# Performance work log

Measured on AMD Instinct MI355X. Metric: run time of the kernel, lower is better.

## Reference

```python
import jax, jax.numpy as jnp
import numpy as np

D_MODEL = 1024
D_HEAD = 64


def setup_inputs() -> dict:
    key = jax.random.key(0)
    ks = jax.random.split(key, 7)
    scale = 1.0 / np.sqrt(D_MODEL)
    x = jax.random.normal(ks[0], (4, 2048, D_MODEL), dtype=jnp.float32)
    Wq = jax.random.normal(ks[1], (D_MODEL, D_HEAD), dtype=jnp.float32) * scale
    bq = jax.random.normal(ks[2], (D_HEAD,), dtype=jnp.float32) * 0.01
    Wk = jax.random.normal(ks[3], (D_MODEL, D_HEAD), dtype=jnp.float32) * scale
    bk = jax.random.normal(ks[4], (D_HEAD,), dtype=jnp.float32) * 0.01
    Wv = jax.random.normal(ks[5], (D_MODEL, D_HEAD), dtype=jnp.float32) * scale
    bv = jax.random.normal(ks[6], (D_HEAD,), dtype=jnp.float32) * 0.01
    return {"x": x, "Wq": Wq, "bq": bq, "Wk": Wk, "bk": bk, "Wv": Wv, "bv": bv}


def reference(x, Wq, bq, Wk, bk, Wv, bv):
    # x: [B, S, d_model]
    seq_len = x.shape[1]
    q = x @ Wq + bq  # [B, S, d_head]
    k = x @ Wk + bk
    v = x @ Wv + bv
    scores = jnp.einsum('bqd,bkd->bqk', q, k) * (1.0 / np.sqrt(D_HEAD))
    causal_mask = jnp.triu(jnp.ones((seq_len, seq_len), dtype=bool), k=1)
    scores = jnp.where(causal_mask, -jnp.inf, scores)
    weights = jax.nn.softmax(scores, axis=-1)  # dropout p=0.0 -> identity
    out = jnp.einsum('bqk,bkd->bqd', weights, v)  # [B, S, d_head]
    return out
```

## Files before the change

### kernel.cpp

```cpp
#include <hip/hip_runtime.h>
#include <math.h>

#define D_MODEL 1024
#define SEQ     2048
#define BATCH   4
#define NROWS   (BATCH * SEQ)

typedef short bf16x8 __attribute__((ext_vector_type(8)));
typedef float f32x4  __attribute__((ext_vector_type(4)));

static __device__ __forceinline__ unsigned short f2bf(float f) {
    unsigned int x = __float_as_uint(f);
    x += 0x7FFFu + ((x >> 16) & 1u);
    return (unsigned short)(x >> 16);
}

__global__ __launch_bounds__(256) void w_pack(
    const float* __restrict__ Wq, const float* __restrict__ Wk,
    const float* __restrict__ Wv, unsigned short* __restrict__ Wb)
{
    __shared__ float st[64][68];
    const int mat = blockIdx.x >> 4;
    const int k0  = (blockIdx.x & 15) * 64;
    const float* W = (mat == 0) ? Wq : (mat == 1) ? Wk : Wv;
    const int t  = threadIdx.x;
    const int kr = t >> 2, cs = (t & 3) * 16;
#pragma unroll
    for (int i = 0; i < 4; ++i)
        *(float4*)&st[kr][cs + i * 4] = *(const float4*)&W[(size_t)(k0 + kr) * 64 + cs + i * 4];
    __syncthreads();
    const int c = t >> 2, ks = (t & 3) * 16;
    unsigned short tmp[16];
#pragma unroll
    for (int j = 0; j < 16; ++j) tmp[j] = f2bf(st[ks + j][c]);
    *(uint4*)&Wb[(size_t)(mat * 64 + c) * D_MODEL + k0 + ks]     = *(uint4*)&tmp[0];
    *(uint4*)&Wb[(size_t)(mat * 64 + c) * D_MODEL + k0 + ks + 8] = *(uint4*)&tmp[8];
}

__global__ __launch_bounds__(256, 1) void qkv_proj_mfma(
    const float* __restrict__ x, const unsigned short* __restrict__ Wb,
    const float* __restrict__ bq, const float* __restrict__ bk,
    const float* __restrict__ bv,
    unsigned short* __restrict__ qb, unsigned short* __restrict__ kb,
    unsigned short* __restrict__ Vt)
{
    __shared__ float smem[6400];
    unsigned short* A_lds = (unsigned short*)smem;
    unsigned short* B_lds = A_lds + 64 * 72;

    const int tid  = threadIdx.x;
    const int wid  = tid >> 6;
    const int lane = tid & 63;
    const int wr   = wid >> 1;
    const int wc   = wid & 1;
    const int lg   = lane >> 4;
    const int lc   = lane & 15;
    const int m0   = blockIdx.x * 64;
    const int n0   = blockIdx.y * 96;
    const int by   = blockIdx.y;

    f32x4 acc[2][3];
#pragma unroll
    for (int mf = 0; mf < 2; ++mf)
#pragma unroll
        for (int nf = 0; nf < 3; ++nf) acc[mf][nf] = (f32x4){0.f, 0.f, 0.f, 0.f};

    const int arow0 = tid >> 3, ac8 = tid & 7;
    const int brow0 = tid >> 3, bc8 = tid & 7;

    float4 a0[2], a1[2];
    uint4  brg[3];

    {
#pragma unroll
        for (int i = 0; i < 2; ++i) {
            const float* ap = &x[(size_t)(m0 + arow0 + 32 * i) * D_MODEL + ac8 * 8];
            a0[i] = *(const float4*)ap;
            a1[i] = *(const float4*)(ap + 4);
        }
#pragma unroll
        for (int i = 0; i < 3; ++i)
            brg[i] = *(const uint4*)&Wb[(size_t)(n0 + brow0 + 32 * i) * D_MODEL + bc8 * 8];
    }

    for (int it = 0; it < 16; ++it) {
        __syncthreads();
#pragma unroll
        for (int i = 0; i < 2; ++i) {
            unsigned int w0 = f2bf(a0[i].x) | ((unsigned)f2bf(a0[i].y) << 16);
            unsigned int w1 = f2bf(a0[i].z) | ((unsigned)f2bf(a0[i].w) << 16);
            unsigned int w2 = f2bf(a1[i].x) | ((unsigned)f2bf(a1[i].y) << 16);
            unsigned int w3 = f2bf(a1[i].z) | ((unsigned)f2bf(a1[i].w) << 16);
            *(uint4*)&A_lds[(arow0 + 32 * i) * 72 + ac8 * 8] = make_uint4(w0, w1, w2, w3);
        }
#pragma unroll
        for (int i = 0; i < 3; ++i)
            *(uint4*)&B_lds[(brow0 + 32 * i) * 72 + bc8 * 8] = brg[i];
        __syncthreads();

        if (it < 15) {
            const int k0 = (it + 1) * 64;
#pragma unroll
            for (int i = 0; i < 2; ++i) {
                const float* ap = &x[(size_t)(m0 + arow0 + 32 * i) * D_MODEL + k0 + ac8 * 8];
                a0[i] = *(const float4*)ap;
                a1[i] = *(const float4*)(ap + 4);
            }
#pragma unroll
            for (int i = 0; i < 3; ++i)
                brg[i] = *(const uint4*)&Wb[(size_t)(n0 + brow0 + 32 * i) * D_MODEL + k0 + bc8 * 8];
        }

#pragma unroll
        for (int kk = 0; kk < 2; ++kk) {
            bf16x8 af[2], bfr[3];
#pragma unroll
            for (int mf = 0; mf < 2; ++mf)
                af[mf] = *(const bf16x8*)&A_lds[(wr * 32 + mf * 16 + lc) * 72 + kk * 32 + lg * 8];
#pragma unroll
            for (int nf = 0; nf < 3; ++nf)
                bfr[nf] = *(const bf16x8*)&B_lds[(wc * 48 + nf * 16 + lc) * 72 + kk * 32 + lg * 8];
#pragma unroll
            for (int mf = 0; mf < 2; ++mf)
#pragma unroll
                for (int nf = 0; nf < 3; ++nf)
                    acc[mf][nf] = __builtin_amdgcn_mfma_f32_16x16x32_bf16(
                        af[mf], bfr[nf], acc[mf][nf], 0, 0, 0);
        }
    }

    __syncthreads();
    float* st = smem;
#pragma unroll
    for (int mf = 0; mf < 2; ++mf)
#pragma unroll
        for (int nf = 0; nf < 3; ++nf)
#pragma unroll
            for (int r = 0; r < 4; ++r)
                st[(wr * 32 + mf * 16 + lg * 4 + r) * 100 + wc * 48 + nf * 16 + lc] = acc[mf][nf][r];
    __syncthreads();

    unsigned short tmp[16];
    if (by == 0) {
        {
            const int row = tid >> 2, c16 = (tid & 3) * 16;
#pragma unroll
            for (int j = 0; j < 16; ++j)
                tmp[j] = f2bf((st[row * 100 + c16 + j] + bq[c16 + j]) * 0.125f);
            unsigned short* dst = &qb[(size_t)(m0 + row) * 64 + c16];
            *(uint4*)dst       = *(uint4*)&tmp[0];
            *(uint4*)(dst + 8) = *(uint4*)&tmp[8];
        }
        if (tid < 128) {
            const int row = tid >> 1, c16 = (tid & 1) * 16;
#pragma unroll
            for (int j = 0; j < 16; ++j)
                tmp[j] = f2bf(st[row * 100 + 64 + c16 + j] + bk[c16 + j]);
            unsigned short* dst = &kb[(size_t)(m0 + row) * 64 + c16];
            *(uint4*)dst       = *(uint4*)&tmp[0];
            *(uint4*)(dst + 8) = *(uint4*)&tmp[8];
        }
    } else {
        if (tid < 128) {
            const int row = tid >> 1, c16 = (tid & 1) * 16;
#pragma unroll
            for (int j = 0; j < 16; ++j)
                tmp[j] = f2bf(st[row * 100 + c16 + j] + bk[32 + c16 + j]);
            unsigned short* dst = &kb[(size_t)(m0 + row) * 64 + 32 + c16];
            *(uint4*)dst       = *(uint4*)&tmp[0];
            *(uint4*)(dst + 8) = *(uint4*)&tmp[8];
        }
        {
            const int d = tid >> 2, s16 = (tid & 3) * 16;
            const float bs = bv[d];
#pragma unroll
            for (int j = 0; j < 16; ++j)
                tmp[j] = f2bf(st[(s16 + j) * 100 + 32 + d] + bs);
            const int bb = m0 >> 11, seq0 = m0 & 2047;
            unsigned short* dst = &Vt[((size_t)(bb * 64 + d)) * SEQ + seq0 + s16];
            *(uint4*)dst       = *(uint4*)&tmp[0];
            *(uint4*)(dst + 8) = *(uint4*)&tmp[8];
        }
    }
}

__global__ __launch_bounds__(64, 2) void attn_partial(
    const unsigned short* __restrict__ qb, const unsigned short* __restrict__ kb,
    const unsigned short* __restrict__ Vt,
    float* __restrict__ O_part, float* __restrict__ ml)
{
    __shared__ unsigned short P_lds[16 * 72];

    const int qt = blockIdx.x;
    const int ch = blockIdx.y;
    const int b  = blockIdx.z;
    const int lane = threadIdx.x;
    const int lg = lane >> 4, lc = lane & 15;

    int nt = ((qt * 16 + 15 - ch * 512) >> 6) + 1;
    if (nt > 8) nt = 8;
    if (nt <= 0) return;

    const size_t qrow = (size_t)(b * SEQ + qt * 16 + lc);
    bf16x8 qf0 = *(const bf16x8*)&qb[qrow * 64 + lg * 8];
    bf16x8 qf1 = *(const bf16x8*)&qb[qrow * 64 + 32 + lg * 8];

    f32x4 O[4];
#pragma unroll
    for (int df = 0; df < 4; ++df) O[df] = (f32x4){0.f, 0.f, 0.f, 0.f};
    float m[4] = {-1e30f, -1e30f, -1e30f, -1e30f};
    float l[4] = {0.f, 0.f, 0.f, 0.f};

    const int rowbase = qt * 16 + lg * 4;

    bf16x8 kr[8], vr[8];
    {
        const int kb0 = ch * 512;
#pragma unroll
        for (int kf = 0; kf < 4; ++kf) {
            const unsigned short* kp = &kb[((size_t)(b * SEQ + kb0 + kf * 16 + lc)) * 64];
            kr[kf * 2]     = *(const bf16x8*)&kp[lg * 8];
            kr[kf * 2 + 1] = *(const bf16x8*)&kp[32 + lg * 8];
            const unsigned short* vp = &Vt[((size_t)(b * 64 + kf * 16 + lc)) * SEQ + kb0];
            vr[kf * 2]     = *(const bf16x8*)&vp[lg * 8];
            vr[kf * 2 + 1] = *(const bf16x8*)&vp[32 + lg * 8];
        }
    }

    for (int t = 0; t < nt; ++t) {
        const int kb0 = ch * 512 + t * 64;

        f32x4 s[4];
#pragma unroll
        for (int kf = 0; kf < 4; ++kf) {
            f32x4 z = (f32x4){0.f, 0.f, 0.f, 0.f};
            z = __builtin_amdgcn_mfma_f32_16x16x32_bf16(qf0, kr[kf * 2], z, 0, 0, 0);
            s[kf] = __builtin_amdgcn_mfma_f32_16x16x32_bf16(qf1, kr[kf * 2 + 1], z, 0, 0, 0);
        }
        if (t + 1 < nt) {
            const int kb0n = kb0 + 64;
#pragma unroll
            for (int kf = 0; kf < 4; ++kf) {
                const unsigned short* kp = &kb[((size_t)(b * SEQ + kb0n + kf * 16 + lc)) * 64];
                kr[kf * 2]     = *(const bf16x8*)&kp[lg * 8];
                kr[kf * 2 + 1] = *(const bf16x8*)&kp[32 + lg * 8];
            }
        }

#pragma unroll
        for (int r = 0; r < 4; ++r) {
            float tm = -1e30f;
#pragma unroll
            for (int kf = 0; kf < 4; ++kf) {
                float sv = s[kf][r];
                if (kb0 + kf * 16 + lc > rowbase + r) sv = -1e30f;
                s[kf][r] = sv;
                tm = fmaxf(tm, sv);
            }
            tm = fmaxf(tm, __shfl_xor(tm, 1));
            tm = fmaxf(tm, __shfl_xor(tm, 2));
            tm = fmaxf(tm, __shfl_xor(tm, 4));
            tm = fmaxf(tm, __shfl_xor(tm, 8));
            float mn  = fmaxf(m[r], tm);
            float fac = __expf(m[r] - mn);
            float ts  = 0.f;
#pragma unroll
            for (int kf = 0; kf < 4; ++kf) {
                float p = __expf(s[kf][r] - mn);
                ts += p;
                P_lds[(lg * 4 + r) * 72 + kf * 16 + lc] = f2bf(p);
            }
            ts += __shfl_xor(ts, 1);
            ts += __shfl_xor(ts, 2);
            ts += __shfl_xor(ts, 4);
            ts += __shfl_xor(ts, 8);
            l[r] = l[r] * fac + ts;
            m[r] = mn;
            O[0][r] *= fac; O[1][r] *= fac; O[2][r] *= fac; O[3][r] *= fac;
        }

        bf16x8 pf0 = *(const bf16x8*)&P_lds[lc * 72 + lg * 8];
        bf16x8 pf1 = *(const bf16x8*)&P_lds[lc * 72 + 32 + lg * 8];
#pragma unroll
        for (int df = 0; df < 4; ++df) {
            O[df] = __builtin_amdgcn_mfma_f32_16x16x32_bf16(pf0, vr[df * 2],     O[df], 0, 0, 0);
            O[df] = __builtin_amdgcn_mfma_f32_16x16x32_bf16(pf1, vr[df * 2 + 1], O[df], 0, 0, 0);
        }
        if (t + 1 < nt) {
            const int kb0n = kb0 + 64;
#pragma unroll
            for (int df = 0; df < 4; ++df) {
                const unsigned short* vp = &Vt[((size_t)(b * 64 + df * 16 + lc)) * SEQ + kb0n];
                vr[df * 2]     = *(const bf16x8*)&vp[lg * 8];
                vr[df * 2 + 1] = *(const bf16x8*)&vp[32 + lg * 8];
            }
        }
    }

    const int slot = (b * 128 + qt) * 4 + ch;
    float* Op = O_part + (size_t)slot * 1024;
#pragma unroll
    for (int df = 0; df < 4; ++df)
#pragma unroll
        for (int r = 0; r < 4; ++r)
            Op[(lg * 4 + r) * 64 + df * 16 + lc] = O[df][r];
    if (lc == 0) {
#pragma unroll
        for (int r = 0; r < 4; ++r) {
            ml[slot * 32 + lg * 4 + r]      = m[r];
            ml[slot * 32 + 16 + lg * 4 + r] = l[r];
        }
    }
}

__global__ __launch_bounds__(256) void attn_merge(
    const float* __restrict__ O_part, const float* __restrict__ ml,
    float* __restrict__ out)
{
    int idx = blockIdx.x * 256 + threadIdx.x;
    int row = idx >> 5;
    int d0  = (idx & 31) * 2;
    int b = row >> 11, seq = row & 2047;
    int qt = seq >> 4, rl = seq & 15;
    int nc = ((qt * 16 + 15) >> 9) + 1;
    int sb = (b * 128 + qt) * 4;

    float M = -1e30f;
    for (int c = 0; c < nc; ++c) M = fmaxf(M, ml[(sb + c) * 32 + rl]);
    float L = 0.f, o0 = 0.f, o1 = 0.f;
    for (int c = 0; c < nc; ++c) {
        float e = __expf(ml[(sb + c) * 32 + rl] - M);
        L += e * ml[(sb + c) * 32 + 16 + rl];
        const float* Op = O_part + (size_t)(sb + c) * 1024 + rl * 64 + d0;
        o0 += e * Op[0];
        o1 += e * Op[1];
    }
    float inv = 1.f / L;
    *(float2*)&out[(size_t)row * 64 + d0] = make_float2(o0 * inv, o1 * inv);
}

extern "C" void kernel_launch(void* const* d_in, const int* in_sizes, int n_in,
                              void* d_out, int out_size, void* d_ws, size_t ws_size,
                              hipStream_t stream)
{
    (void)in_sizes; (void)n_in; (void)out_size; (void)ws_size;

    const float* x  = (const float*)d_in[0];
    const float* Wq = (const float*)d_in[1];
    const float* bq = (const float*)d_in[2];
    const float* Wk = (const float*)d_in[3];
    const float* bk = (const float*)d_in[4];
    const float* Wv = (const float*)d_in[5];
    const float* bv = (const float*)d_in[6];
    float* out = (float*)d_out;

    char* ws = (char*)d_ws;
    unsigned short* Wb = (unsigned short*)(ws);
    unsigned short* qb = (unsigned short*)(ws + 393216);
    unsigned short* kb = (unsigned short*)(ws + 393216 + 1048576);
    unsigned short* Vt = (unsigned short*)(ws + 393216 + 2 * 1048576);
    float*          ml = (float*)(ws + 393216 + 3 * 1048576);
    float*      O_part = (float*)(ws + 393216 + 3 * 1048576 + 262144);

    w_pack<<<48, 256, 0, stream>>>(Wq, Wk, Wv, Wb);
    qkv_proj_mfma<<<dim3(128, 2), 256, 0, stream>>>(x, Wb, bq, bk, bv, qb, kb, Vt);
    attn_partial<<<dim3(128, 4, 4), 64, 0, stream>>>(qb, kb, Vt, O_part, ml);
    attn_merge<<<1024, 256, 0, stream>>>(O_part, ml, out);
}
```

Baseline: 140.6 us.

## Halve projection tile rows, fold log2e into Q scale, reverse attention block order

The QKV projection now uses 32-row tiles with 128 threads per block, giving 512 blocks instead of 256 so more CUs are busy. Each block now loads the full 96-column weight slice on its own, which raises total weight traffic. Q is pre-scaled by log2(e) so the softmax and merge kernels can call exp2f instead of __expf. The attention partial kernel schedules query tiles in reverse order so the heavy causal tiles start first, which should reduce tail imbalance.

```diff
diff --git a/kernel.cpp b/kernel.cpp
--- a/kernel.cpp
+++ b/kernel.cpp
@@ -37,25 +37,23 @@
     *(uint4*)&Wb[(size_t)(mat * 64 + c) * D_MODEL + k0 + ks + 8] = *(uint4*)&tmp[8];
 }
 
-__global__ __launch_bounds__(256, 1) void qkv_proj_mfma(
+__global__ __launch_bounds__(128, 2) void qkv_proj_mfma(
     const float* __restrict__ x, const unsigned short* __restrict__ Wb,
     const float* __restrict__ bq, const float* __restrict__ bk,
     const float* __restrict__ bv,
     unsigned short* __restrict__ qb, unsigned short* __restrict__ kb,
     unsigned short* __restrict__ Vt)
 {
-    __shared__ float smem[6400];
+    __shared__ float smem[4608];
     unsigned short* A_lds = (unsigned short*)smem;
-    unsigned short* B_lds = A_lds + 64 * 72;
+    unsigned short* B_lds = A_lds + 32 * 72;
 
     const int tid  = threadIdx.x;
-    const int wid  = tid >> 6;
+    const int wc   = tid >> 6;
     const int lane = tid & 63;
-    const int wr   = wid >> 1;
-    const int wc   = wid & 1;
     const int lg   = lane >> 4;
     const int lc   = lane & 15;
-    const int m0   = blockIdx.x * 64;
+    const int m0   = blockIdx.x * 32;
     const int n0   = blockIdx.y * 96;
     const int by   = blockIdx.y;
 
@@ -65,22 +63,20 @@
 #pragma unroll
         for (int nf = 0; nf < 3; ++nf) acc[mf][nf] = (f32x4){0.f, 0.f, 0.f, 0.f};
 
-    const int arow0 = tid >> 3, ac8 = tid & 7;
-    const int brow0 = tid >> 3, bc8 = tid & 7;
-
+    const int arow = tid >> 3, ac8 = tid & 7;
     float4 a0[2], a1[2];
-    uint4  brg[3];
+    uint4  brg[6];
 
     {
 #pragma unroll
         for (int i = 0; i < 2; ++i) {
-            const float* ap = &x[(size_t)(m0 + arow0 + 32 * i) * D_MODEL + ac8 * 8];
+            const float* ap = &x[(size_t)(m0 + arow + 16 * i) * D_MODEL + ac8 * 8];
             a0[i] = *(const float4*)ap;
             a1[i] = *(const float4*)(ap + 4);
         }
 #pragma unroll
-        for (int i = 0; i < 3; ++i)
-            brg[i] = *(const uint4*)&Wb[(size_t)(n0 + brow0 + 32 * i) * D_MODEL + bc8 * 8];
+        for (int i = 0; i < 6; ++i)
+            brg[i] = *(const uint4*)&Wb[(size_t)(n0 + arow + 16 * i) * D_MODEL + ac8 * 8];
     }
 
     for (int it = 0; it < 16; ++it) {
@@ -91,24 +87,24 @@
             unsigned int w1 = f2bf(a0[i].z) | ((unsigned)f2bf(a0[i].w) << 16);
             unsigned int w2 = f2bf(a1[i].x) | ((unsigned)f2bf(a1[i].y) << 16);
             unsigned int w3 = f2bf(a1[i].z) | ((unsigned)f2bf(a1[i].w) << 16);
-            *(uint4*)&A_lds[(arow0 + 32 * i) * 72 + ac8 * 8] = make_uint4(w0, w1, w2, w3);
-        }
-#pragma unroll
-        for (int i = 0; i < 3; ++i)
-            *(uint4*)&B_lds[(brow0 + 32 * i) * 72 + bc8 * 8] = brg[i];
+            *(uint4*)&A_lds[(arow + 16 * i) * 72 + ac8 * 8] = make_uint4(w0, w1, w2, w3);
+        }
+#pragma unroll
+        for (int i = 0; i < 6; ++i)
+            *(uint4*)&B_lds[(arow + 16 * i) * 72 + ac8 * 8] = brg[i];
         __syncthreads();
 
         if (it < 15) {
             const int k0 = (it + 1) * 64;
 #pragma unroll
             for (int i = 0; i < 2; ++i) {
-                const float* ap = &x[(size_t)(m0 + arow0 + 32 * i) * D_MODEL + k0 + ac8 * 8];
+                const float* ap = &x[(size_t)(m0 + arow + 16 * i) * D_MODEL + k0 + ac8 * 8];
                 a0[i] = *(const float4*)ap;
                 a1[i] = *(const float4*)(ap + 4);
             }
 #pragma unroll
-            for (int i = 0; i < 3; ++i)
-                brg[i] = *(const uint4*)&Wb[(size_t)(n0 + brow0 + 32 * i) * D_MODEL + k0 + bc8 * 8];
+            for (int i = 0; i < 6; ++i)
+                brg[i] = *(const uint4*)&Wb[(size_t)(n0 + arow + 16 * i) * D_MODEL + k0 + ac8 * 8];
         }
 
 #pragma unroll
@@ -116,7 +112,7 @@
             bf16x8 af[2], bfr[3];
 #pragma unroll
             for (int mf = 0; mf < 2; ++mf)
-                af[mf] = *(const bf16x8*)&A_lds[(wr * 32 + mf * 16 + lc) * 72 + kk * 32 + lg * 8];
+                af[mf] = *(const bf16x8*)&A_lds[(mf * 16 + lc) * 72 + kk * 32 + lg * 8];
 #pragma unroll
             for (int nf = 0; nf < 3; ++nf)
                 bfr[nf] = *(const bf16x8*)&B_lds[(wc * 48 + nf * 16 + lc) * 72 + kk * 32 + lg * 8];
@@ -137,21 +133,22 @@
         for (int nf = 0; nf < 3; ++nf)
 #pragma unroll
             for (int r = 0; r < 4; ++r)
-                st[(wr * 32 + mf * 16 + lg * 4 + r) * 100 + wc * 48 + nf * 16 + lc] = acc[mf][nf][r];
+                st[(mf * 16 + lg * 4 + r) * 100 + wc * 48 + nf * 16 + lc] = acc[mf][nf][r];
     __syncthreads();
 
     unsigned short tmp[16];
+    const float QSCALE = 0.125f * 1.4426950408889634f;
     if (by == 0) {
         {
             const int row = tid >> 2, c16 = (tid & 3) * 16;
 #pragma unroll
             for (int j = 0; j < 16; ++j)
-                tmp[j] = f2bf((st[row * 100 + c16 + j] + bq[c16 + j]) * 0.125f);
+                tmp[j] = f2bf((st[row * 100 + c16 + j] + bq[c16 + j]) * QSCALE);
             unsigned short* dst = &qb[(size_t)(m0 + row) * 64 + c16];
             *(uint4*)dst       = *(uint4*)&tmp[0];
             *(uint4*)(dst + 8) = *(uint4*)&tmp[8];
         }
-        if (tid < 128) {
+        if (tid < 64) {
             const int row = tid >> 1, c16 = (tid & 1) * 16;
 #pragma unroll
             for (int j = 0; j < 16; ++j)
@@ -161,7 +158,7 @@
             *(uint4*)(dst + 8) = *(uint4*)&tmp[8];
         }
     } else {
-        if (tid < 128) {
+        if (tid < 64) {
             const int row = tid >> 1, c16 = (tid & 1) * 16;
 #pragma unroll
             for (int j = 0; j < 16; ++j)
@@ -171,7 +168,7 @@
             *(uint4*)(dst + 8) = *(uint4*)&tmp[8];
         }
         {
-            const int d = tid >> 2, s16 = (tid & 3) * 16;
+            const int d = tid >> 1, s16 = (tid & 1) * 16;
             const float bs = bv[d];
 #pragma unroll
             for (int j = 0; j < 16; ++j)
@@ -191,7 +188,7 @@
 {
     __shared__ unsigned short P_lds[16 * 72];
 
-    const int qt = blockIdx.x;
+    const int qt = (int)gridDim.x - 1 - (int)blockIdx.x;
     const int ch = blockIdx.y;
     const int b  = blockIdx.z;
     const int lane = threadIdx.x;
@@ -262,11 +259,11 @@
             tm = fmaxf(tm, __shfl_xor(tm, 4));
             tm = fmaxf(tm, __shfl_xor(tm, 8));
             float mn  = fmaxf(m[r], tm);
-            float fac = __expf(m[r] - mn);
+            float fac = exp2f(m[r] - mn);
             float ts  = 0.f;
 #pragma unroll
             for (int kf = 0; kf < 4; ++kf) {
-                float p = __expf(s[kf][r] - mn);
+                float p = exp2f(s[kf][r] - mn);
                 ts += p;
                 P_lds[(lg * 4 + r) * 72 + kf * 16 + lc] = f2bf(p);
             }
@@ -329,7 +326,7 @@
     for (int c = 0; c < nc; ++c) M = fmaxf(M, ml[(sb + c) * 32 + rl]);
     float L = 0.f, o0 = 0.f, o1 = 0.f;
     for (int c = 0; c < nc; ++c) {
-        float e = __expf(ml[(sb + c) * 32 + rl] - M);
+        float e = exp2f(ml[(sb + c) * 32 + rl] - M);
         L += e * ml[(sb + c) * 32 + 16 + rl];
         const float* Op = O_part + (size_t)(sb + c) * 1024 + rl * 64 + d0;
         o0 += e * Op[0];
@@ -363,7 +360,7 @@
     float*      O_part = (float*)(ws + 393216 + 3 * 1048576 + 262144);
 
     w_pack<<<48, 256, 0, stream>>>(Wq, Wk, Wv, Wb);
-    qkv_proj_mfma<<<dim3(128, 2), 256, 0, stream>>>(x, Wb, bq, bk, bv, qb, kb, Vt);
+    qkv_proj_mfma<<<dim3(256, 2), 128, 0, stream>>>(x, Wb, bq, bk, bv, qb, kb, Vt);
     attn_partial<<<dim3(128, 4, 4), 64, 0, stream>>>(qb, kb, Vt, O_part, ml);
     attn_merge<<<1024, 256, 0, stream>>>(O_part, ml, out);
 }
```

Measured after the change: 151.3 us. 7.6% more time.
